# Kernel optimization log

Hardware: AMD Instinct MI355X
Metric: run time of the kernel (lower is better)

The kernel has to match this reference:

```python
import jax, jax.numpy as jnp
import numpy as np

GROUPS = 4
RATIO = 2


def setup_inputs() -> dict:
    key = jax.random.key(0)
    k1, k2, k3 = jax.random.split(key, 3)
    B, C, H, W = 16, 256, 64, 64
    c_out = 2 * GROUPS * RATIO ** 2  # 32
    x = jax.random.normal(k1, (B, C, H, W), dtype=jnp.float32)
    # offset conv: normal_init std=0.001 (full 1x1 conv)
    w_off = jax.random.normal(k2, (c_out, C), dtype=jnp.float32) * 0.001
    b_off = jnp.zeros((c_out,), dtype=jnp.float32)
    # scope conv: grouped 1x1 (groups=4); init is zeros in the module, use tiny
    # random values so sigmoid != exactly 0.5 and the path is exercised
    w_scope = jax.random.normal(k3, (GROUPS, c_out // GROUPS, C // GROUPS), dtype=jnp.float32) * 0.001
    b_scope = jnp.zeros((c_out,), dtype=jnp.float32)
    return {"x": x, "w_off": w_off, "b_off": b_off, "w_scope": w_scope, "b_scope": b_scope}


def _pixel_shuffle(t, r):
    B, C, H, W = t.shape
    Co = C // (r * r)
    t = t.reshape(B, Co, r, r, H, W)
    t = t.transpose(0, 1, 4, 2, 5, 3)  # B, Co, H, r, W, r
    return t.reshape(B, Co, H * r, W * r)


def _bilinear_border(img, ix, iy):
    # img: (c, H, W); ix, iy: (Ho, Wo) pixel coords in input space
    c, H, W = img.shape
    ix = jnp.clip(ix, 0.0, W - 1.0)  # border padding: clamp coordinate
    iy = jnp.clip(iy, 0.0, H - 1.0)
    x0f = jnp.floor(ix)
    y0f = jnp.floor(iy)
    wx = ix - x0f
    wy = iy - y0f
    x0 = jnp.clip(x0f.astype(jnp.int32), 0, W - 1)
    x1 = jnp.clip(x0 + 1, 0, W - 1)
    y0 = jnp.clip(y0f.astype(jnp.int32), 0, H - 1)
    y1 = jnp.clip(y0 + 1, 0, H - 1)
    v00 = img[:, y0, x0]
    v01 = img[:, y0, x1]
    v10 = img[:, y1, x0]
    v11 = img[:, y1, x1]
    return (v00 * (1 - wy) * (1 - wx) + v01 * (1 - wy) * wx
            + v10 * wy * (1 - wx) + v11 * wy * wx)


def reference(x, w_off, b_off, w_scope, b_scope):
    B, C, H, W = x.shape
    g, r = GROUPS, RATIO
    # offset 1x1 conv
    off = jnp.einsum('bihw,oi->bohw', x, w_off) + b_off[None, :, None, None]
    # grouped scope 1x1 conv + sigmoid scaling
    xgc = x.reshape(B, g, C // g, H, W)
    sc = jnp.einsum('bgihw,goi->bgohw', xgc, w_scope).reshape(B, -1, H, W)
    sc = sc + b_scope[None, :, None, None]
    off = jax.nn.sigmoid(sc) * 0.5 * off
    # pixel shuffle to (B, 2*g, Ho, Wo)
    off = _pixel_shuffle(off, r)
    Ho, Wo = H * r, W * r
    # rearrange: x 'b (c grp) h w -> (b grp) c h w'; offset 'b (grp two) h w -> (b grp) h w two'
    cg = C // g
    xg = x.reshape(B, cg, g, H, W).transpose(0, 2, 1, 3, 4).reshape(B * g, cg, H, W)
    og = off.reshape(B, g, 2, Ho, Wo).transpose(0, 1, 3, 4, 2).reshape(B * g, Ho, Wo, 2)
    # sampling grid: centers + offset, normalized by (Wo, Ho), align_corners=False
    posx = jnp.linspace(0.5, Wo - 0.5, Wo, dtype=x.dtype)[None, :]   # (1, Wo)
    posy = jnp.linspace(0.5, Ho - 0.5, Ho, dtype=x.dtype)[:, None]   # (Ho, 1)
    gx = 2.0 * (posx + og[..., 0]) / Wo - 1.0  # (B*g, Ho, Wo)
    gy = 2.0 * (posy + og[..., 1]) / Ho - 1.0
    # unnormalize (align_corners=False): pix = ((g+1)*size - 1) / 2
    ix = ((gx + 1.0) * W - 1.0) * 0.5
    iy = ((gy + 1.0) * H - 1.0) * 0.5
    out = jax.vmap(_bilinear_border)(xg, ix, iy)  # (B*g, cg, Ho, Wo)
    # rearrange back: '(b grp) c h w -> b (c grp) h w'
    out = out.reshape(B, g, cg, Ho, Wo).transpose(0, 2, 1, 3, 4).reshape(B, C, Ho, Wo)
    return out
```

## Files before the change

### kernel.cpp

```cpp
#include <hip/hip_runtime.h>
#include <math.h>

#define B_   16
#define C_   256
#define H_   64
#define W_   64
#define G_   4
#define HO_  128
#define WO_  128
#define HW_  (H_ * W_)
#define HOWO_ (HO_ * WO_)

__constant__ float wconst[8 * 32 * 40];

__global__ __launch_bounds__(256) void prep_kernel(
    const float* __restrict__ w_off,
    const float* __restrict__ w_scope,
    float* __restrict__ wout)
{
    const int k = blockIdx.x * 256 + threadIdx.x;
    if (k >= 8 * 32 * 40) return;
    const int q  = k % 40;
    const int r  = k / 40;
    const int i2 = r & 31;
    const int u  = r >> 5;
    const int v  = u & 3;
    const int hi = u >> 2;
    const int i  = 64 * v + 32 * hi + i2;
    float val;
    if (q < 32) val = w_off[q * 256 + i];
    else        val = w_scope[v * 512 + (q - 32) * 64 + 32 * hi + i2];
    wout[k] = val;
}

__global__ __launch_bounds__(512, 6) void fused_kernel(
    const float* __restrict__ x,
    const float* __restrict__ b_off,
    const float* __restrict__ b_scope,
    float* __restrict__ out)
{
    __shared__ float4 red[8][8][64];
    __shared__ float4 aux[8][64];

    const int tid = threadIdx.x;
    const int u   = __builtin_amdgcn_readfirstlane(tid >> 6);
    const int w   = tid & 63;
    const int v   = u & 3;
    const int hi  = u >> 2;
    const int h   = blockIdx.x & 63;
    const int b   = blockIdx.x >> 6;

    const float* xq = x + (size_t)b * C_ * HW_ +
                      (size_t)(64 * v + 32 * hi) * HW_ + h * W_ + w;
    const int wbase0 = u * (32 * 40);

    float offp[32];
    float scp[8];
#pragma unroll
    for (int j = 0; j < 32; ++j) offp[j] = 0.f;
#pragma unroll
    for (int j = 0; j < 8; ++j) scp[j] = 0.f;

#pragma unroll 4
    for (int i2 = 0; i2 < 32; ++i2) {
        const float xv = xq[(size_t)i2 * HW_];
        const int wb = wbase0 + i2 * 40;
#pragma unroll
        for (int j = 0; j < 32; ++j) offp[j] += xv * wconst[wb + j];
#pragma unroll
        for (int j = 0; j < 8; ++j)  scp[j] += xv * wconst[wb + 32 + j];
    }

    if (hi) {
#pragma unroll
        for (int j = 0; j < 8; ++j)
            red[4 + v][j][w] = make_float4(offp[4 * j + 0], offp[4 * j + 1],
                                           offp[4 * j + 2], offp[4 * j + 3]);
        aux[2 * v + 0][w] = make_float4(scp[0], scp[1], scp[2], scp[3]);
        aux[2 * v + 1][w] = make_float4(scp[4], scp[5], scp[6], scp[7]);
    }
    __syncthreads();
    if (!hi) {
#pragma unroll
        for (int j = 0; j < 8; ++j) {
            const float4 p = red[4 + v][j][w];
            offp[4 * j + 0] += p.x; offp[4 * j + 1] += p.y;
            offp[4 * j + 2] += p.z; offp[4 * j + 3] += p.w;
        }
        const float4 s0 = aux[2 * v + 0][w];
        const float4 s1 = aux[2 * v + 1][w];
        scp[0] += s0.x; scp[1] += s0.y; scp[2] += s0.z; scp[3] += s0.w;
        scp[4] += s1.x; scp[5] += s1.y; scp[6] += s1.z; scp[7] += s1.w;
#pragma unroll
        for (int j = 0; j < 8; ++j)
            red[v][j][w] = make_float4(offp[4 * j + 0], offp[4 * j + 1],
                                       offp[4 * j + 2], offp[4 * j + 3]);
    }
    __syncthreads();
    if (!hi) {
        float4 a = make_float4(0.f, 0.f, 0.f, 0.f);
        float4 c = make_float4(0.f, 0.f, 0.f, 0.f);
#pragma unroll
        for (int tt = 0; tt < 4; ++tt) {
            const float4 pa = red[tt][2 * v + 0][w];
            const float4 pc = red[tt][2 * v + 1][w];
            a.x += pa.x; a.y += pa.y; a.z += pa.z; a.w += pa.w;
            c.x += pc.x; c.y += pc.y; c.z += pc.z; c.w += pc.w;
        }
        const float ao[8] = {a.x, a.y, a.z, a.w, c.x, c.y, c.z, c.w};
        float f[8];
#pragma unroll
        for (int j = 0; j < 8; ++j) {
            const float offv = ao[j] + b_off[8 * v + j];
            const float scv  = scp[j] + b_scope[8 * v + j];
            f[j] = offv * 0.5f / (1.f + expf(-scv));
        }
#pragma unroll
        for (int r1 = 0; r1 < 2; ++r1) {
            const float hoF = (float)(2 * h + r1);
            float ix0 = ((float)(2 * w + 0) - 0.5f + f[2 * r1 + 0]) * 0.5f;
            float iy0 = (hoF - 0.5f + f[4 + 2 * r1 + 0]) * 0.5f;
            float ix1 = ((float)(2 * w + 1) - 0.5f + f[2 * r1 + 1]) * 0.5f;
            float iy1 = (hoF - 0.5f + f[4 + 2 * r1 + 1]) * 0.5f;
            ix0 = fminf(fmaxf(ix0, 0.f), (float)(W_ - 1));
            iy0 = fminf(fmaxf(iy0, 0.f), (float)(H_ - 1));
            ix1 = fminf(fmaxf(ix1, 0.f), (float)(W_ - 1));
            iy1 = fminf(fmaxf(iy1, 0.f), (float)(H_ - 1));
            aux[2 * v + r1][w] = make_float4(ix0, iy0, ix1, iy1);
        }
    }
    __syncthreads();

    const int wo = tid & 127;
    const int z  = (tid >> 7) & 1;
    const int gh = tid >> 8;
    const int ho = 2 * h + z;

    const float2* cbase = (const float2*)&aux[0][0];
    const float* xb0 = x + (size_t)b * C_ * HW_;
    float* ob0 = out + (size_t)b * C_ * HOWO_ + ho * WO_ + wo;

#pragma unroll
    for (int gg = 0; gg < 2; ++gg) {
        const int g = 2 * gh + gg;
        const float2 c = cbase[(g * 2 + z) * 128 + wo];
        const float ix = c.x, iy = c.y;

        const float x0f = floorf(ix);
        const float y0f = floorf(iy);
        const float wx = ix - x0f;
        const float wy = iy - y0f;
        int x0 = (int)x0f;
        int y0 = (int)y0f;
        x0 = max(0, min(x0, W_ - 1));
        y0 = max(0, min(y0, H_ - 1));
        const int x1 = min(x0 + 1, W_ - 1);
        const int y1 = min(y0 + 1, H_ - 1);

        const float w00 = (1.f - wy) * (1.f - wx);
        const float w01 = (1.f - wy) * wx;
        const float w10 = wy * (1.f - wx);
        const float w11 = wy * wx;

        const int p00 = y0 * W_ + x0;
        const int p01 = y0 * W_ + x1;
        const int p10 = y1 * W_ + x0;
        const int p11 = y1 * W_ + x1;

        const float* xb = xb0 + (size_t)g * HW_;
        float* ob = ob0 + (size_t)g * HOWO_;

#pragma unroll 4
        for (int cc = 0; cc < 64; ++cc) {
            const float* pl = xb + (size_t)cc * 4 * HW_;
            const float val = pl[p00] * w00 + pl[p01] * w01 +
                              pl[p10] * w10 + pl[p11] * w11;
            ob[(size_t)cc * 4 * HOWO_] = val;
        }
    }
}

extern "C" void kernel_launch(void* const* d_in, const int* in_sizes, int n_in,
                              void* d_out, int out_size, void* d_ws, size_t ws_size,
                              hipStream_t stream) {
    const float* x       = (const float*)d_in[0];
    const float* w_off   = (const float*)d_in[1];
    const float* b_off   = (const float*)d_in[2];
    const float* w_scope = (const float*)d_in[3];
    const float* b_scope = (const float*)d_in[4];
    float* out = (float*)d_out;

    void* wsym = nullptr;
    (void)hipGetSymbolAddress(&wsym, HIP_SYMBOL(wconst));

    prep_kernel<<<dim3(40), 256, 0, stream>>>(w_off, w_scope, (float*)wsym);
    fused_kernel<<<dim3(B_ * H_), 512, 0, stream>>>(x, b_off, b_scope, out);
}
```

Measured before the change: 93.41 us.

## Split each input row across two blocks by output sub-row to double grid parallelism

Each block now handles one of the two output sub-rows (z) for an input row, computing only the 16 offset and 4 scope channels that sub-row needs. This halves the per-thread accumulator registers and lets launch bounds rise to 8 waves, and the grid doubles to 2048 blocks. Block IDs are swizzled so neighbouring blocks work on different regions. The cost is that the x channel reads for the 1x1 conv are duplicated across the two blocks that share an input row.

```diff
diff --git a/kernel.cpp b/kernel.cpp
--- a/kernel.cpp
+++ b/kernel.cpp
@@ -11,7 +11,7 @@
 #define HW_  (H_ * W_)
 #define HOWO_ (HO_ * WO_)
 
-__constant__ float wconst[8 * 32 * 40];
+__constant__ float wconst[2 * 8 * 32 * 20];
 
 __global__ __launch_bounds__(256) void prep_kernel(
     const float* __restrict__ w_off,
@@ -19,164 +19,161 @@
     float* __restrict__ wout)
 {
     const int k = blockIdx.x * 256 + threadIdx.x;
-    if (k >= 8 * 32 * 40) return;
-    const int q  = k % 40;
-    const int r  = k / 40;
+    if (k >= 2 * 8 * 32 * 20) return;
+    const int q  = k % 20;
+    const int r  = k / 20;
     const int i2 = r & 31;
-    const int u  = r >> 5;
+    const int u  = (r >> 5) & 7;
+    const int z  = r >> 8;
     const int v  = u & 3;
     const int hi = u >> 2;
     const int i  = 64 * v + 32 * hi + i2;
     float val;
-    if (q < 32) val = w_off[q * 256 + i];
-    else        val = w_scope[v * 512 + (q - 32) * 64 + 32 * hi + i2];
+    if (q < 16) {
+        const int vv = q >> 2, k4 = q & 3;
+        const int j  = (k4 & 1) + 2 * z + 4 * (k4 >> 1);
+        val = w_off[(8 * vv + j) * 256 + i];
+    } else {
+        const int k4 = q - 16;
+        const int j  = (k4 & 1) + 2 * z + 4 * (k4 >> 1);
+        val = w_scope[v * 512 + j * 64 + 32 * hi + i2];
+    }
     wout[k] = val;
 }
 
-__global__ __launch_bounds__(512, 6) void fused_kernel(
+__global__ __launch_bounds__(512, 8) void fused_kernel(
     const float* __restrict__ x,
     const float* __restrict__ b_off,
     const float* __restrict__ b_scope,
     float* __restrict__ out)
 {
-    __shared__ float4 red[8][8][64];
-    __shared__ float4 aux[8][64];
+    __shared__ float4 red[8][4][64];
+    __shared__ float4 auxs[4][64];
+    __shared__ float4 coordbuf[4][64];
 
     const int tid = threadIdx.x;
     const int u   = __builtin_amdgcn_readfirstlane(tid >> 6);
     const int w   = tid & 63;
+
+    const int bid = ((blockIdx.x & 7) << 8) | (blockIdx.x >> 3);
+    const int z   = bid & 1;
+    const int h   = (bid >> 1) & 63;
+    const int b   = bid >> 7;
+
     const int v   = u & 3;
     const int hi  = u >> 2;
-    const int h   = blockIdx.x & 63;
-    const int b   = blockIdx.x >> 6;
 
     const float* xq = x + (size_t)b * C_ * HW_ +
                       (size_t)(64 * v + 32 * hi) * HW_ + h * W_ + w;
-    const int wbase0 = u * (32 * 40);
+    const int wbase0 = (z * 8 + u) * (32 * 20);
 
-    float offp[32];
-    float scp[8];
+    float offp[16];
+    float scp[4];
 #pragma unroll
-    for (int j = 0; j < 32; ++j) offp[j] = 0.f;
+    for (int j = 0; j < 16; ++j) offp[j] = 0.f;
 #pragma unroll
-    for (int j = 0; j < 8; ++j) scp[j] = 0.f;
+    for (int j = 0; j < 4; ++j) scp[j] = 0.f;
 
 #pragma unroll 4
     for (int i2 = 0; i2 < 32; ++i2) {
         const float xv = xq[(size_t)i2 * HW_];
-        const int wb = wbase0 + i2 * 40;
+        const int wb = wbase0 + i2 * 20;
 #pragma unroll
-        for (int j = 0; j < 32; ++j) offp[j] += xv * wconst[wb + j];
+        for (int j = 0; j < 16; ++j) offp[j] += xv * wconst[wb + j];
 #pragma unroll
-        for (int j = 0; j < 8; ++j)  scp[j] += xv * wconst[wb + 32 + j];
+        for (int j = 0; j < 4; ++j)  scp[j] += xv * wconst[wb + 16 + j];
     }
 
     if (hi) {
 #pragma unroll
-        for (int j = 0; j < 8; ++j)
-            red[4 + v][j][w] = make_float4(offp[4 * j + 0], offp[4 * j + 1],
-                                           offp[4 * j + 2], offp[4 * j + 3]);
-        aux[2 * v + 0][w] = make_float4(scp[0], scp[1], scp[2], scp[3]);
-        aux[2 * v + 1][w] = make_float4(scp[4], scp[5], scp[6], scp[7]);
+        for (int c = 0; c < 4; ++c)
+            red[u][c][w] = make_float4(offp[4 * c + 0], offp[4 * c + 1],
+                                       offp[4 * c + 2], offp[4 * c + 3]);
+        auxs[v][w] = make_float4(scp[0], scp[1], scp[2], scp[3]);
     }
     __syncthreads();
     if (!hi) {
 #pragma unroll
-        for (int j = 0; j < 8; ++j) {
-            const float4 p = red[4 + v][j][w];
-            offp[4 * j + 0] += p.x; offp[4 * j + 1] += p.y;
-            offp[4 * j + 2] += p.z; offp[4 * j + 3] += p.w;
+        for (int c = 0; c < 4; ++c) {
+            const float4 p = red[u + 4][c][w];
+            offp[4 * c + 0] += p.x; offp[4 * c + 1] += p.y;
+            offp[4 * c + 2] += p.z; offp[4 * c + 3] += p.w;
         }
-        const float4 s0 = aux[2 * v + 0][w];
-        const float4 s1 = aux[2 * v + 1][w];
+        const float4 s0 = auxs[v][w];
         scp[0] += s0.x; scp[1] += s0.y; scp[2] += s0.z; scp[3] += s0.w;
-        scp[4] += s1.x; scp[5] += s1.y; scp[6] += s1.z; scp[7] += s1.w;
 #pragma unroll
-        for (int j = 0; j < 8; ++j)
-            red[v][j][w] = make_float4(offp[4 * j + 0], offp[4 * j + 1],
-                                       offp[4 * j + 2], offp[4 * j + 3]);
+        for (int c = 0; c < 4; ++c)
+            red[u][c][w] = make_float4(offp[4 * c + 0], offp[4 * c + 1],
+                                       offp[4 * c + 2], offp[4 * c + 3]);
     }
     __syncthreads();
     if (!hi) {
         float4 a = make_float4(0.f, 0.f, 0.f, 0.f);
-        float4 c = make_float4(0.f, 0.f, 0.f, 0.f);
 #pragma unroll
         for (int tt = 0; tt < 4; ++tt) {
-            const float4 pa = red[tt][2 * v + 0][w];
-            const float4 pc = red[tt][2 * v + 1][w];
+            const float4 pa = red[tt][v][w];
             a.x += pa.x; a.y += pa.y; a.z += pa.z; a.w += pa.w;
-            c.x += pc.x; c.y += pc.y; c.z += pc.z; c.w += pc.w;
         }
-        const float ao[8] = {a.x, a.y, a.z, a.w, c.x, c.y, c.z, c.w};
-        float f[8];
+        const float ao[4] = {a.x, a.y, a.z, a.w};
+        float f[4];
 #pragma unroll
-        for (int j = 0; j < 8; ++j) {
-            const float offv = ao[j] + b_off[8 * v + j];
-            const float scv  = scp[j] + b_scope[8 * v + j];
-            f[j] = offv * 0.5f / (1.f + expf(-scv));
+        for (int k = 0; k < 4; ++k) {
+            const int j = (k & 1) + 2 * z + 4 * (k >> 1);
+            const float offv = ao[k] + b_off[8 * v + j];
+            const float scv  = scp[k] + b_scope[8 * v + j];
+            f[k] = offv * 0.5f / (1.f + expf(-scv));
         }
-#pragma unroll
-        for (int r1 = 0; r1 < 2; ++r1) {
-            const float hoF = (float)(2 * h + r1);
-            float ix0 = ((float)(2 * w + 0) - 0.5f + f[2 * r1 + 0]) * 0.5f;
-            float iy0 = (hoF - 0.5f + f[4 + 2 * r1 + 0]) * 0.5f;
-            float ix1 = ((float)(2 * w + 1) - 0.5f + f[2 * r1 + 1]) * 0.5f;
-            float iy1 = (hoF - 0.5f + f[4 + 2 * r1 + 1]) * 0.5f;
-            ix0 = fminf(fmaxf(ix0, 0.f), (float)(W_ - 1));
-            iy0 = fminf(fmaxf(iy0, 0.f), (float)(H_ - 1));
-            ix1 = fminf(fmaxf(ix1, 0.f), (float)(W_ - 1));
-            iy1 = fminf(fmaxf(iy1, 0.f), (float)(H_ - 1));
-            aux[2 * v + r1][w] = make_float4(ix0, iy0, ix1, iy1);
-        }
+        const float hoF = (float)(2 * h + z);
+        float ix0 = ((float)(2 * w + 0) - 0.5f + f[0]) * 0.5f;
+        float iy0 = (hoF - 0.5f + f[2]) * 0.5f;
+        float ix1 = ((float)(2 * w + 1) - 0.5f + f[1]) * 0.5f;
+        float iy1 = (hoF - 0.5f + f[3]) * 0.5f;
+        ix0 = fminf(fmaxf(ix0, 0.f), (float)(W_ - 1));
+        iy0 = fminf(fmaxf(iy0, 0.f), (float)(H_ - 1));
+        ix1 = fminf(fmaxf(ix1, 0.f), (float)(W_ - 1));
+        iy1 = fminf(fmaxf(iy1, 0.f), (float)(H_ - 1));
+        coordbuf[v][w] = make_float4(ix0, iy0, ix1, iy1);
     }
     __syncthreads();
 
     const int wo = tid & 127;
-    const int z  = (tid >> 7) & 1;
-    const int gh = tid >> 8;
+    const int g  = tid >> 7;
     const int ho = 2 * h + z;
 
-    const float2* cbase = (const float2*)&aux[0][0];
-    const float* xb0 = x + (size_t)b * C_ * HW_;
-    float* ob0 = out + (size_t)b * C_ * HOWO_ + ho * WO_ + wo;
+    const float2 c = ((const float2*)&coordbuf[g][0])[wo];
+    const float ix = c.x, iy = c.y;
 
-#pragma unroll
-    for (int gg = 0; gg < 2; ++gg) {
-        const int g = 2 * gh + gg;
-        const float2 c = cbase[(g * 2 + z) * 128 + wo];
-        const float ix = c.x, iy = c.y;
+    const float x0f = floorf(ix);
+    const float y0f = floorf(iy);
+    const float wx = ix - x0f;
+    const float wy = iy - y0f;
+    int x0 = (int)x0f;
+    int y0 = (int)y0f;
+    x0 = max(0, min(x0, W_ - 1));
+    y0 = max(0, min(y0, H_ - 1));
+    const int x1 = min(x0 + 1, W_ - 1);
+    const int y1 = min(y0 + 1, H_ - 1);
 
-        const float x0f = floorf(ix);
-        const float y0f = floorf(iy);
-        const float wx = ix - x0f;
-        const float wy = iy - y0f;
-        int x0 = (int)x0f;
-        int y0 = (int)y0f;
-        x0 = max(0, min(x0, W_ - 1));
-        y0 = max(0, min(y0, H_ - 1));
-        const int x1 = min(x0 + 1, W_ - 1);
-        const int y1 = min(y0 + 1, H_ - 1);
+    const float w00 = (1.f - wy) * (1.f - wx);
+    const float w01 = (1.f - wy) * wx;
+    const float w10 = wy * (1.f - wx);
+    const float w11 = wy * wx;
 
-        const float w00 = (1.f - wy) * (1.f - wx);
-        const float w01 = (1.f - wy) * wx;
-        const float w10 = wy * (1.f - wx);
-        const float w11 = wy * wx;
+    const int p00 = y0 * W_ + x0;
+    const int p01 = y0 * W_ + x1;
+    const int p10 = y1 * W_ + x0;
+    const int p11 = y1 * W_ + x1;
 
-        const int p00 = y0 * W_ + x0;
-        const int p01 = y0 * W_ + x1;
-        const int p10 = y1 * W_ + x0;
-        const int p11 = y1 * W_ + x1;
-
-        const float* xb = xb0 + (size_t)g * HW_;
-        float* ob = ob0 + (size_t)g * HOWO_;
+    const float* xb = x + (size_t)b * C_ * HW_ + (size_t)g * HW_;
+    float* ob = out + (size_t)b * C_ * HOWO_ + (size_t)g * HOWO_ +
+                ho * WO_ + wo;
 
 #pragma unroll 4
-        for (int cc = 0; cc < 64; ++cc) {
-            const float* pl = xb + (size_t)cc * 4 * HW_;
-            const float val = pl[p00] * w00 + pl[p01] * w01 +
-                              pl[p10] * w10 + pl[p11] * w11;
-            ob[(size_t)cc * 4 * HOWO_] = val;
-        }
+    for (int cc = 0; cc < 64; ++cc) {
+        const float* pl = xb + (size_t)cc * 4 * HW_;
+        const float val = pl[p00] * w00 + pl[p01] * w01 +
+                          pl[p10] * w10 + pl[p11] * w11;
+        ob[(size_t)cc * 4 * HOWO_] = val;
     }
 }
 
@@ -194,5 +191,5 @@
     (void)hipGetSymbolAddress(&wsym, HIP_SYMBOL(wconst));
 
     prep_kernel<<<dim3(40), 256, 0, stream>>>(w_off, w_scope, (float*)wsym);
-    fused_kernel<<<dim3(B_ * H_), 512, 0, stream>>>(x, b_off, b_scope, out);
+    fused_kernel<<<dim3(2 * B_ * H_), 512, 0, stream>>>(x, b_off, b_scope, out);
 }
```

After: 99.77 us. 6.8% more time.
